# Optimization experiments

Hardware: AMD Instinct MI355X
Metric: run time of the kernel (lower is better)

The kernel has to match this reference:

```python
import jax, jax.numpy as jnp
import numpy as np

EPS = 1e-5

def setup_inputs() -> dict:
    key = jax.random.key(0)
    ks = jax.random.split(key, 4)
    B, C, H, W = 8, 512, 64, 64
    K, V = 64, 512
    x = jax.random.normal(ks[0], (B, C, H, W), dtype=jnp.float32)
    Wq = jax.random.normal(ks[1], (K, C), dtype=jnp.float32) * (1.0 / np.sqrt(C))
    bq = jnp.zeros((K,), dtype=jnp.float32)
    Wk = jax.random.normal(ks[2], (K, C), dtype=jnp.float32) * (1.0 / np.sqrt(C))
    bk = jnp.zeros((K,), dtype=jnp.float32)
    Wv = jax.random.normal(ks[3], (V, C), dtype=jnp.float32) * (1.0 / np.sqrt(C))
    bn_gamma = jnp.ones((V,), dtype=jnp.float32)
    bn_beta = jnp.zeros((V,), dtype=jnp.float32)
    bn_mean = jnp.zeros((V,), dtype=jnp.float32)
    bn_var = jnp.ones((V,), dtype=jnp.float32)
    return {"x": x, "Wq": Wq, "bq": bq, "Wk": Wk, "bk": bk, "Wv": Wv,
            "bn_gamma": bn_gamma, "bn_beta": bn_beta,
            "bn_mean": bn_mean, "bn_var": bn_var}

def reference(x, Wq, bq, Wk, bk, Wv, bn_gamma, bn_beta, bn_mean, bn_var):
    B, C, H, W = x.shape
    N = H * W
    xf = x.reshape(B, C, N)                      # B,C,N
    # 1x1 convs == channel matmuls
    q = jnp.einsum('kc,bcn->bnk', Wq, xf) + bq   # B,N,K  (proj_query permuted)
    k = jnp.einsum('kc,bcn->bkn', Wk, xf) + bk[None, :, None]  # B,K,N
    energy = jnp.einsum('bnk,bkm->bnm', q, k)    # B,N,N
    attention = jax.nn.softmax(energy, axis=-1)  # B,N,N
    # value branch: conv1x1 (no bias) -> BN (inference) -> ReLU
    v = jnp.einsum('vc,bcn->bvn', Wv, xf)        # B,V,N
    scale = bn_gamma / jnp.sqrt(bn_var + EPS)
    shift = bn_beta - bn_mean * scale
    v = jax.nn.relu(v * scale[None, :, None] + shift[None, :, None])
    # out = V @ attention^T
    out = jnp.einsum('bvm,bnm->bvn', v, attention)  # B,V,N
    return out.reshape(B, C, H, W)
```

## Files before the change

### kernel.cpp

```cpp
#include <hip/hip_runtime.h>

typedef __attribute__((ext_vector_type(8))) _Float16 half8;
typedef __attribute__((ext_vector_type(4))) float f32x4;

#define BN_EPS 1e-5f
#define LOG2E 1.4426950408889634f

__device__ __forceinline__ void async_copy16(const void* g, void* l) {
  __builtin_amdgcn_global_load_lds((const __attribute__((address_space(1))) void*)g,
                                   (__attribute__((address_space(3))) void*)l,
                                   16, 0, 0);
}

__global__ void k_transpose(const float* __restrict__ x, _Float16* __restrict__ xT) {
  __shared__ float tile[64][65];
  int n0 = blockIdx.x * 64, c0 = blockIdx.y * 64, b = blockIdx.z;
  const float* xb = x + (size_t)b * 512 * 4096;
  int t = threadIdx.x;
#pragma unroll
  for (int rep = 0; rep < 16; ++rep) {
    int idx = rep * 256 + t;
    int r = idx >> 6, cc = idx & 63;
    tile[r][cc] = xb[(size_t)(c0 + r) * 4096 + n0 + cc];
  }
  __syncthreads();
  _Float16* xTb = xT + (size_t)b * 4096 * 512;
#pragma unroll
  for (int rep = 0; rep < 16; ++rep) {
    int idx = rep * 256 + t;
    int r = idx >> 6, cc = idx & 63;
    xTb[(size_t)(n0 + r) * 512 + c0 + cc] = (_Float16)tile[cc][r];
  }
}

__global__ void k_wall(const float* __restrict__ Wq, const float* __restrict__ Wk,
                       const float* __restrict__ Wv, _Float16* __restrict__ W_all) {
  int i = blockIdx.x * 256 + threadIdx.x;
  if (i >= 640 * 512) return;
  int m = i >> 9, c = i & 511;
  float v;
  if (m < 64) v = Wq[m * 512 + c];
  else if (m < 128) v = Wk[(m - 64) * 512 + c];
  else v = Wv[(m - 128) * 512 + c];
  W_all[i] = (_Float16)v;
}

__global__ __launch_bounds__(256) void k_proj(
    const _Float16* __restrict__ W_all, const _Float16* __restrict__ xT,
    const float* __restrict__ bq, const float* __restrict__ bk,
    const float* __restrict__ gamma, const float* __restrict__ beta,
    const float* __restrict__ mean, const float* __restrict__ var,
    _Float16* __restrict__ q_buf, _Float16* __restrict__ kT_buf,
    _Float16* __restrict__ v_buf) {
  __shared__ __align__(16) _Float16 A_lds[128 * 32];
  __shared__ __align__(16) _Float16 B_lds[128 * 32];
  int nt = blockIdx.x, mt = blockIdx.y, b = blockIdx.z;
  int t = threadIdx.x, w = t >> 6, lane = t & 63;
  int quad = lane >> 4, l16 = lane & 15;
  int moff = (w & 1) * 64, noff = (w >> 1) * 64;

  f32x4 acc[4][4] = {};

  for (int kk = 0; kk < 16; ++kk) {
    int kc = kk * 32;
#pragma unroll
    for (int c = 0; c < 2; ++c) {
      int row = (w * 2 + c) * 16 + (lane >> 2);
      int kseg = (lane & 3) * 8;
      async_copy16(W_all + (size_t)(mt * 128 + row) * 512 + kc + kseg,
                   (char*)A_lds + (w * 2 + c) * 1024 + lane * 16);
      async_copy16(xT + ((size_t)b * 4096 + nt * 128 + row) * 512 + kc + kseg,
                   (char*)B_lds + (w * 2 + c) * 1024 + lane * 16);
    }
    __syncthreads();
    half8 a[4], bb[4];
#pragma unroll
    for (int mi = 0; mi < 4; ++mi)
      a[mi] = *(const half8*)&A_lds[(moff + 16 * mi + l16) * 32 + 8 * quad];
#pragma unroll
    for (int ni = 0; ni < 4; ++ni)
      bb[ni] = *(const half8*)&B_lds[(noff + 16 * ni + l16) * 32 + 8 * quad];
#pragma unroll
    for (int mi = 0; mi < 4; ++mi)
#pragma unroll
      for (int ni = 0; ni < 4; ++ni)
        acc[mi][ni] = __builtin_amdgcn_mfma_f32_16x16x32_f16(a[mi], bb[ni], acc[mi][ni], 0, 0, 0);
    __syncthreads();
  }

  size_t bN = (size_t)b * 4096;
#pragma unroll
  for (int mi = 0; mi < 4; ++mi) {
    int mbase = mt * 128 + moff + 16 * mi + 4 * quad;
#pragma unroll
    for (int ni = 0; ni < 4; ++ni) {
      int n = nt * 128 + noff + 16 * ni + l16;
#pragma unroll
      for (int i = 0; i < 4; ++i) {
        int m = mbase + i;
        float val = acc[mi][ni][i];
        if (m < 64) {
          q_buf[(bN + n) * 64 + m] = (_Float16)((val + bq[m]) * LOG2E);
        } else if (m < 128) {
          kT_buf[(bN + n) * 64 + (m - 64)] = (_Float16)(val + bk[m - 64]);
        } else {
          int vv = m - 128;
          float sc = gamma[vv] * rsqrtf(var[vv] + BN_EPS);
          float sh = beta[vv] - mean[vv] * sc;
          float r = val * sc + sh;
          v_buf[((size_t)b * 512 + vv) * 4096 + n] = (_Float16)(r > 0.f ? r : 0.f);
        }
      }
    }
  }
}

__global__ __launch_bounds__(512, 2) void k_flash(
    const _Float16* __restrict__ q_buf, const _Float16* __restrict__ kT_buf,
    const _Float16* __restrict__ v_buf, float* __restrict__ out) {
  __shared__ __align__(16) _Float16 P_lds[2][128 * 72];
  __shared__ __align__(16) _Float16 K_lds[2][64 * 64];
  __shared__ __align__(16) float alpha_lds[2][128];
  __shared__ __align__(16) float l_lds[128];
  int bx = blockIdx.x;
  int b = bx & 7;
  int n0 = (bx >> 3) * 128;
  int t = threadIdx.x, w = t >> 6, lane = t & 63, quad = lane >> 4, l16 = lane & 15;
  const _Float16* qb = q_buf + (size_t)b * 4096 * 64;
  const char* kbb = (const char*)(kT_buf + (size_t)b * 4096 * 64);
  const _Float16* vp = v_buf + (size_t)b * 512 * 4096 + (size_t)(64 * w + l16) * 4096 + 8 * quad;

  bool pv_first = (w >= 4);

  int st_r = w * 8 + (lane >> 3);
  int st_c = (lane & 7) ^ (st_r & 7);
  int st_dst = w * 1024 + lane * 16;
  int st_src = st_r * 128 + st_c * 16;

  half8 aq[2];
#pragma unroll
  for (int s = 0; s < 2; ++s)
    aq[s] = *(const half8*)&qb[(size_t)(n0 + 16 * w + l16) * 64 + 32 * s + 8 * quad];

  f32x4 o[8][4] = {};
  float m_st[4], l_st[4];
#pragma unroll
  for (int i = 0; i < 4; ++i) { m_st[i] = -1e30f; l_st[i] = 0.f; }

  auto qk_softmax = [&](const _Float16* Kb, _Float16* Pb, float* Ab) {
    f32x4 sc[4];
    __builtin_amdgcn_s_setprio(1);
#pragma unroll
    for (int ct = 0; ct < 4; ++ct) {
      int row = 16 * ct + l16;
      int sw = (row & 7) * 16;
      half8 k0 = *(const half8*)((const char*)Kb + row * 128 + ((quad * 16) ^ sw));
      half8 k1 = *(const half8*)((const char*)Kb + row * 128 + (((4 + quad) * 16) ^ sw));
      f32x4 sa = {0.f, 0.f, 0.f, 0.f};
      sa = __builtin_amdgcn_mfma_f32_16x16x32_f16(aq[0], k0, sa, 0, 0, 0);
      sa = __builtin_amdgcn_mfma_f32_16x16x32_f16(aq[1], k1, sa, 0, 0, 0);
      sc[ct] = sa;
    }
    __builtin_amdgcn_s_setprio(0);
#pragma unroll
    for (int i = 0; i < 4; ++i) {
      float mxi = fmaxf(fmaxf(sc[0][i], sc[1][i]), fmaxf(sc[2][i], sc[3][i]));
#pragma unroll
      for (int off = 1; off < 16; off <<= 1) mxi = fmaxf(mxi, __shfl_xor(mxi, off));
      float mnew = (mxi > m_st[i] + 8.f) ? mxi : m_st[i];
      float alpha_i = exp2f(m_st[i] - mnew);
      m_st[i] = mnew;
      float rsum = 0.f;
#pragma unroll
      for (int ct = 0; ct < 4; ++ct) {
        float pv = exp2f(sc[ct][i] - mnew);
        Pb[(16 * w + 4 * quad + i) * 72 + 16 * ct + l16] = (_Float16)pv;
        rsum += pv;
      }
      l_st[i] = l_st[i] * alpha_i + rsum;
      if (l16 == 0) Ab[16 * w + 4 * quad + i] = alpha_i;
    }
  };

  auto rescale = [&](const float* Ab) {
#pragma unroll
    for (int rt = 0; rt < 8; ++rt) {
      f32x4 ar = *(const f32x4*)&Ab[16 * rt + 4 * quad];
      bool nd = (ar[0] != 1.f) | (ar[1] != 1.f) | (ar[2] != 1.f) | (ar[3] != 1.f);
      if (__any(nd)) {
#pragma unroll
        for (int c2 = 0; c2 < 4; ++c2)
#pragma unroll
          for (int i = 0; i < 4; ++i) o[rt][c2][i] *= ar[i];
      }
    }
  };

  half8 vreg[8];
  auto pv_step = [&](const _Float16* Pb, int mn) {
    __builtin_amdgcn_s_setprio(1);
#pragma unroll
    for (int rt = 0; rt < 8; ++rt) {
      half8 pa0 = *(const half8*)&Pb[(16 * rt + l16) * 72 + 8 * quad];
      half8 pa1 = *(const half8*)&Pb[(16 * rt + l16) * 72 + 32 + 8 * quad];
#pragma unroll
      for (int c2 = 0; c2 < 4; ++c2) {
        o[rt][c2] = __builtin_amdgcn_mfma_f32_16x16x32_f16(pa0, vreg[2 * c2], o[rt][c2], 0, 0, 0);
        o[rt][c2] = __builtin_amdgcn_mfma_f32_16x16x32_f16(pa1, vreg[2 * c2 + 1], o[rt][c2], 0, 0, 0);
      }
    }
    __builtin_amdgcn_s_setprio(0);
#pragma unroll
    for (int c2 = 0; c2 < 4; ++c2) {
      vreg[2 * c2]     = *(const half8*)&vp[c2 * 65536 + mn];
      vreg[2 * c2 + 1] = *(const half8*)&vp[c2 * 65536 + mn + 32];
    }
  };

#pragma unroll
  for (int c2 = 0; c2 < 4; ++c2)
#pragma unroll
    for (int s = 0; s < 2; ++s)
      vreg[2 * c2 + s] = *(const half8*)&vp[c2 * 65536 + 32 * s];
  async_copy16(kbb + st_src, (char*)K_lds[0] + st_dst);
  async_copy16(kbb + 64 * 128 + st_src, (char*)K_lds[1] + st_dst);
  __syncthreads();
  qk_softmax(K_lds[0], P_lds[0], alpha_lds[0]);

#pragma unroll 1
  for (int it = 0; it < 63; ++it) {
    int cur = it & 1, nxt = cur ^ 1;
    __syncthreads();
    int ms = (it + 2 < 64 ? it + 2 : 63) * 64;
    async_copy16(kbb + (size_t)ms * 128 + st_src, (char*)K_lds[cur] + st_dst);
    rescale(alpha_lds[cur]);
    if (pv_first) {
      pv_step(P_lds[cur], (it + 1) * 64);
      qk_softmax(K_lds[nxt], P_lds[nxt], alpha_lds[nxt]);
    } else {
      qk_softmax(K_lds[nxt], P_lds[nxt], alpha_lds[nxt]);
      pv_step(P_lds[cur], (it + 1) * 64);
    }
  }
  __syncthreads();
  rescale(alpha_lds[1]);
  pv_step(P_lds[1], 63 * 64);

#pragma unroll
  for (int i = 0; i < 4; ++i) {
    float s = l_st[i];
#pragma unroll
    for (int off = 1; off < 16; off <<= 1) s += __shfl_xor(s, off);
    if (l16 == 0) l_lds[16 * w + 4 * quad + i] = s;
  }
  __syncthreads();
  float* ob = out + (size_t)b * 512 * 4096;
#pragma unroll
  for (int rt = 0; rt < 8; ++rt) {
    f32x4 lv = *(const f32x4*)&l_lds[16 * rt + 4 * quad];
    f32x4 inv;
#pragma unroll
    for (int i = 0; i < 4; ++i) inv[i] = 1.0f / lv[i];
#pragma unroll
    for (int c2 = 0; c2 < 4; ++c2) {
      int vv = 64 * w + 16 * c2 + l16;
      f32x4 res = o[rt][c2] * inv;
      *(f32x4*)(ob + (size_t)vv * 4096 + n0 + 16 * rt + 4 * quad) = res;
    }
  }
}

extern "C" void kernel_launch(void* const* d_in, const int* in_sizes, int n_in,
                              void* d_out, int out_size, void* d_ws, size_t ws_size,
                              hipStream_t stream) {
  const float* x     = (const float*)d_in[0];
  const float* Wq    = (const float*)d_in[1];
  const float* bq    = (const float*)d_in[2];
  const float* Wk    = (const float*)d_in[3];
  const float* bk    = (const float*)d_in[4];
  const float* Wv    = (const float*)d_in[5];
  const float* gamma = (const float*)d_in[6];
  const float* beta  = (const float*)d_in[7];
  const float* mean  = (const float*)d_in[8];
  const float* var   = (const float*)d_in[9];
  float* out = (float*)d_out;

  char* ws = (char*)d_ws;
  _Float16* xT     = (_Float16*)(ws);
  _Float16* W_all  = (_Float16*)(ws + 33554432);
  _Float16* q_buf  = (_Float16*)(ws + 34209792);
  _Float16* kT_buf = (_Float16*)(ws + 38404096);
  _Float16* v_buf  = (_Float16*)(ws + 42598400);

  k_transpose<<<dim3(64, 8, 8), 256, 0, stream>>>(x, xT);
  k_wall<<<dim3(1280), 256, 0, stream>>>(Wq, Wk, Wv, W_all);
  k_proj<<<dim3(32, 5, 8), 256, 0, stream>>>(W_all, xT, bq, bk, gamma, beta, mean, var,
                                             q_buf, kT_buf, v_buf);
  k_flash<<<dim3(256), 512, 0, stream>>>(q_buf, kT_buf, v_buf, out);
}
```

Measured before the change: 400.4 us.

## Double-buffer projection GEMM LDS loads and vectorize transpose kernel

The projection GEMM now uses two LDS buffers and issues the async global-to-LDS copy for the next k-slice before computing on the current one. This lets load latency overlap with MFMA work instead of stalling at a barrier every iteration. The transpose kernel is also rewritten to use 16-byte float4 global reads and 8-byte half4 writes, replacing scalar accesses. The cost is doubled LDS use in k_proj, and correctness depends on a barrier sitting in the right place in the part of the loop that is not shown.

```diff
diff --git a/kernel.cpp b/kernel.cpp
--- a/kernel.cpp
+++ b/kernel.cpp
@@ -1,6 +1,7 @@
 #include <hip/hip_runtime.h>
 
 typedef __attribute__((ext_vector_type(8))) _Float16 half8;
+typedef __attribute__((ext_vector_type(4))) _Float16 half4;
 typedef __attribute__((ext_vector_type(4))) float f32x4;
 
 #define BN_EPS 1e-5f
@@ -12,24 +13,32 @@
                                    16, 0, 0);
 }
 
-__global__ void k_transpose(const float* __restrict__ x, _Float16* __restrict__ xT) {
+__global__ __launch_bounds__(256) void k_transpose(const float* __restrict__ x,
+                                                   _Float16* __restrict__ xT) {
   __shared__ float tile[64][65];
   int n0 = blockIdx.x * 64, c0 = blockIdx.y * 64, b = blockIdx.z;
   const float* xb = x + (size_t)b * 512 * 4096;
   int t = threadIdx.x;
 #pragma unroll
-  for (int rep = 0; rep < 16; ++rep) {
-    int idx = rep * 256 + t;
-    int r = idx >> 6, cc = idx & 63;
-    tile[r][cc] = xb[(size_t)(c0 + r) * 4096 + n0 + cc];
+  for (int rep = 0; rep < 4; ++rep) {
+    int f = rep * 256 + t;
+    int c = f >> 4, n4 = f & 15;
+    f32x4 v = *(const f32x4*)&xb[(size_t)(c0 + c) * 4096 + n0 + n4 * 4];
+    tile[c][n4 * 4 + 0] = v[0];
+    tile[c][n4 * 4 + 1] = v[1];
+    tile[c][n4 * 4 + 2] = v[2];
+    tile[c][n4 * 4 + 3] = v[3];
   }
   __syncthreads();
   _Float16* xTb = xT + (size_t)b * 4096 * 512;
 #pragma unroll
-  for (int rep = 0; rep < 16; ++rep) {
-    int idx = rep * 256 + t;
-    int r = idx >> 6, cc = idx & 63;
-    xTb[(size_t)(n0 + r) * 512 + c0 + cc] = (_Float16)tile[cc][r];
+  for (int rep = 0; rep < 4; ++rep) {
+    int g = rep * 256 + t;
+    int n = g >> 4, c4 = g & 15;
+    half4 h;
+#pragma unroll
+    for (int j = 0; j < 4; ++j) h[j] = (_Float16)tile[c4 * 4 + j][n];
+    *(half4*)&xTb[(size_t)(n0 + n) * 512 + c0 + c4 * 4] = h;
   }
 }
 
@@ -52,8 +61,8 @@
     const float* __restrict__ mean, const float* __restrict__ var,
     _Float16* __restrict__ q_buf, _Float16* __restrict__ kT_buf,
     _Float16* __restrict__ v_buf) {
-  __shared__ __align__(16) _Float16 A_lds[128 * 32];
-  __shared__ __align__(16) _Float16 B_lds[128 * 32];
+  __shared__ __align__(16) _Float16 A_lds[2][128 * 32];
+  __shared__ __align__(16) _Float16 B_lds[2][128 * 32];
   int nt = blockIdx.x, mt = blockIdx.y, b = blockIdx.z;
   int t = threadIdx.x, w = t >> 6, lane = t & 63;
   int quad = lane >> 4, l16 = lane & 15;
@@ -61,25 +70,33 @@
 
   f32x4 acc[4][4] = {};
 
-  for (int kk = 0; kk < 16; ++kk) {
+  auto stage = [&](int kk, int buf) {
     int kc = kk * 32;
 #pragma unroll
     for (int c = 0; c < 2; ++c) {
       int row = (w * 2 + c) * 16 + (lane >> 2);
       int kseg = (lane & 3) * 8;
       async_copy16(W_all + (size_t)(mt * 128 + row) * 512 + kc + kseg,
-                   (char*)A_lds + (w * 2 + c) * 1024 + lane * 16);
+                   (char*)A_lds[buf] + (w * 2 + c) * 1024 + lane * 16);
       async_copy16(xT + ((size_t)b * 4096 + nt * 128 + row) * 512 + kc + kseg,
-                   (char*)B_lds + (w * 2 + c) * 1024 + lane * 16);
-    }
-    __syncthreads();
+                   (char*)B_lds[buf] + (w * 2 + c) * 1024 + lane * 16);
+    }
+  };
+
+  stage(0, 0);
+  __syncthreads();
+
+#pragma unroll 1
+  for (int kk = 0; kk < 16; ++kk) {
+    int cur = kk & 1;
+    if (kk < 15) stage(kk + 1, cur ^ 1);
     half8 a[4], bb[4];
 #pragma unroll
     for (int mi = 0; mi < 4; ++mi)
-      a[mi] = *(const half8*)&A_lds[(moff + 16 * mi + l16) * 32 + 8 * quad];
+      a[mi] = *(const half8*)&A_lds[cur][(moff + 16 * mi + l16) * 32 + 8 * quad];
 #pragma unroll
     for (int ni = 0; ni < 4; ++ni)
-      bb[ni] = *(const half8*)&B_lds[(noff + 16 * ni + l16) * 32 + 8 * quad];
+      bb[ni] = *(const half8*)&B_lds[cur][(noff + 16 * ni + l16) * 32 + 8 * quad];
 #pragma unroll
     for (int mi = 0; mi < 4; ++mi)
 #pragma unroll
```

New measurement: 388.4 us. 3.0% less time.
